# Performance work log

Hardware: AMD Instinct MI355X
Metric: run time of the kernel (lower is better)

Reference implementation:

```python
import jax, jax.numpy as jnp
import numpy as np
from jax import lax

# dims: B batch, L seq len, D channels, N SSM state size
BATCH, L, D, N = 8, 2048, 256, 64
MIN_DELTA = 1e-6
EPS = 1e-6


def setup_inputs() -> dict:
    key = jax.random.key(0)
    k0, k1, k2, k3, k4 = jax.random.split(key, 5)
    x = jax.random.normal(k0, (BATCH, L, D), dtype=jnp.float32)
    # log_A chosen so A = softplus(log_A) is small -> discrete_A^L stays finite in fp32
    log_A = -jax.random.normal(k1, (N, N), dtype=jnp.float32) - 3.0
    Bp = jax.random.normal(k2, (D, N), dtype=jnp.float32) * 0.02
    Cp = jax.random.normal(k3, (D, N), dtype=jnp.float32) * 0.02
    log_delta = jnp.full((D,), -8.0, dtype=jnp.float32)  # dt ~ 3.4e-4 (stability)
    skip_D = jnp.ones((D,), dtype=jnp.float32)
    W_out = jax.random.normal(k4, (D, D), dtype=jnp.float32) * (1.0 / np.sqrt(D))
    b_out = jnp.zeros((D,), dtype=jnp.float32)
    return dict(x=x, log_A=log_A, Bp=Bp, Cp=Cp, log_delta=log_delta,
                skip_D=skip_D, W_out=W_out, b_out=b_out)


def reference(x, log_A, Bp, Cp, log_delta, skip_D, W_out, b_out):
    Bsz, Lx, Dx = x.shape
    # --- discretize ---
    A = jax.nn.softplus(log_A)                                  # [N,N]
    dt = jax.nn.softplus(log_delta) + MIN_DELTA                 # [D]
    dA = jax.vmap(jax.scipy.linalg.expm)(A[None] * dt[:, None, None])  # [D,N,N]
    I = jnp.eye(A.shape[0], dtype=A.dtype)
    X = jnp.linalg.solve(A + EPS * I, Bp.T)                     # [N,D] = A^{-1} B^T
    dB = jnp.einsum('dnm,dm->dn', dA - I, X.T)                  # [D,N]
    # --- kernel k[d,l] = C_d . (dA_d)^l dB_d, via sequential recurrence (same math
    # as the explicit A-power loop, carrying the vector instead of the matrix) ---
    def step(v, _):
        return jnp.einsum('dnm,dm->dn', dA, v), jnp.sum(Cp * v, axis=-1)
    _, ks = lax.scan(step, dB, None, length=Lx)                 # ks: [L,D]
    k = ks.T                                                    # [D,L]
    # --- grouped causal conv1d: y[b,d,t] = sum_tau k[d,tau] x[b,d,t-tau] ---
    w = jnp.flip(k, -1)[:, None, :]                             # [D,1,L]
    y = lax.conv_general_dilated(
        jnp.transpose(x, (0, 2, 1)), w, (1,), [(Lx - 1, 0)],
        dimension_numbers=('NCH', 'OIH', 'NCH'), feature_group_count=Dx)
    y = jnp.transpose(y, (0, 2, 1))                             # [B,L,D]
    return (y + x * skip_D) @ W_out.T + b_out
```

## Files before the change

kernel.cpp:

```cpp
#include <hip/hip_runtime.h>

#define Bz 8
#define Lz 2048
#define Dz 256
#define Nz 64
#define SP 68
#define SA 65
#define SAK 72
#define SKB 136
#define KE 4
#define KP 7
#define BSP 4
#define BPB (Bz / BSP)

typedef __attribute__((ext_vector_type(8))) short bf16x8;
typedef __attribute__((ext_vector_type(4))) float f32x4;

__device__ __forceinline__ float softplusf(float x) {
  return (x > 20.f) ? x : log1pf(expf(x));
}

__device__ __forceinline__ unsigned short f2bf(float f) {
  unsigned int u = __float_as_uint(f);
  u += 0x7fffu + ((u >> 16) & 1u);
  return (unsigned short)(u >> 16);
}

__device__ __forceinline__ void pmm_acc(const float* __restrict__ LA,
                                        const float* __restrict__ LB,
                                        float* acc, int n, int q) {
  float arow[64];
#pragma unroll
  for (int mm = 0; mm < 16; ++mm) {
    const float4 a4 = *(const float4*)(LA + n * SP + mm * 4);
    arow[4 * mm + 0] = a4.x; arow[4 * mm + 1] = a4.y;
    arow[4 * mm + 2] = a4.z; arow[4 * mm + 3] = a4.w;
  }
#pragma unroll
  for (int i = 0; i < 16; ++i) acc[i] = 0.f;
#pragma unroll 8
  for (int m = 0; m < 64; ++m) {
    const float4 b0 = *(const float4*)(LB + m * SP + q * 16 + 0);
    const float4 b1 = *(const float4*)(LB + m * SP + q * 16 + 4);
    const float4 b2 = *(const float4*)(LB + m * SP + q * 16 + 8);
    const float4 b3 = *(const float4*)(LB + m * SP + q * 16 + 12);
    const float a = arow[m];
    acc[0]  = fmaf(a, b0.x, acc[0]);  acc[1]  = fmaf(a, b0.y, acc[1]);
    acc[2]  = fmaf(a, b0.z, acc[2]);  acc[3]  = fmaf(a, b0.w, acc[3]);
    acc[4]  = fmaf(a, b1.x, acc[4]);  acc[5]  = fmaf(a, b1.y, acc[5]);
    acc[6]  = fmaf(a, b1.z, acc[6]);  acc[7]  = fmaf(a, b1.w, acc[7]);
    acc[8]  = fmaf(a, b2.x, acc[8]);  acc[9]  = fmaf(a, b2.y, acc[9]);
    acc[10] = fmaf(a, b2.z, acc[10]); acc[11] = fmaf(a, b2.w, acc[11]);
    acc[12] = fmaf(a, b3.x, acc[12]); acc[13] = fmaf(a, b3.y, acc[13]);
    acc[14] = fmaf(a, b3.z, acc[14]); acc[15] = fmaf(a, b3.w, acc[15]);
  }
}

__global__ __launch_bounds__(256) void s4_xt(const float* __restrict__ x,
                                             float* __restrict__ xT,
                                             const float* __restrict__ log_A,
                                             float* __restrict__ Apow) {
  if (blockIdx.x == 0 && blockIdx.y == 0) {
    const int i = blockIdx.z * 512 + threadIdx.x;
    Apow[i] = softplusf(log_A[i]);
    Apow[i + 256] = softplusf(log_A[i + 256]);
  }
  __shared__ float tile[64][69];
  const int t0 = blockIdx.x * 64, d0 = blockIdx.y * 64, b = blockIdx.z;
  const int rr = threadIdx.x >> 4;
  const int c4 = (threadIdx.x & 15) * 4;
#pragma unroll
  for (int p = 0; p < 4; ++p) {
    const int row = p * 16 + rr;
    const float4 v = *(const float4*)(x + ((size_t)b * Lz + t0 + row) * Dz + d0 + c4);
    tile[row][c4 + 0] = v.x; tile[row][c4 + 1] = v.y;
    tile[row][c4 + 2] = v.z; tile[row][c4 + 3] = v.w;
  }
  __syncthreads();
#pragma unroll
  for (int p = 0; p < 4; ++p) {
    const int dd = p * 16 + rr;
    float4 o;
    o.x = tile[c4 + 0][dd]; o.y = tile[c4 + 1][dd];
    o.z = tile[c4 + 2][dd]; o.w = tile[c4 + 3][dd];
    *(float4*)(xT + ((size_t)(d0 + dd) * Bz + b) * Lz + t0 + c4) = o;
  }
}

__global__ __launch_bounds__(256, 1) void s4_buildpow(
    float* __restrict__ Apow, const float* __restrict__ Bp,
    const float* __restrict__ Cp, const float* __restrict__ log_delta,
    float* __restrict__ Gk, float* __restrict__ Qk,
    float* __restrict__ kloc, float* __restrict__ dts) {
  __shared__ float As[Nz * SA];
  __shared__ float Pst[KP + 1][Nz];
  __shared__ float Qst[KE + 1][Nz];
  __shared__ float Pv[Nz], Qv[Nz], dBs[Nz];
  __shared__ float prA[4][Nz + 8], prB[4][Nz + 8];
  __shared__ float zp[KE + 1][17], zs[KE + 1];
  __shared__ alignas(16) float PA[Nz * SP];
  __shared__ alignas(16) float PB[Nz * SP];
  const int tid = threadIdx.x;
  const int d = blockIdx.x;
  const int n = tid & 63, qq = tid >> 6;

  if (d >= Dz) {
    const int role = d - Dz;
#pragma unroll
    for (int i = 0; i < 4; ++i) {
      const int e = (tid + 256 * i) * 4;
      const int r = e >> 6, c = e & 63;
      const float4 v = *(const float4*)(Apow + e);
      *(float4*)&PA[r * SP + c] = v;
      *(float4*)&PB[r * SP + c] = v;
    }
    __syncthreads();
    float acc[16];
    pmm_acc(PA, PB, acc, n, qq);
    if (role == 0) {
      float* O = Apow + (size_t)1 * 4096;
#pragma unroll
      for (int v = 0; v < 4; ++v) {
        float4 o;
        o.x = acc[4 * v]; o.y = acc[4 * v + 1];
        o.z = acc[4 * v + 2]; o.w = acc[4 * v + 3];
        *(float4*)(O + n * 64 + qq * 16 + 4 * v) = o;
      }
      return;
    }
    __syncthreads();
#pragma unroll
    for (int i = 0; i < 16; ++i) {
      PB[n * SP + qq * 16 + i] = acc[i];
      if (role == 2) PA[n * SP + qq * 16 + i] = acc[i];
    }
    __syncthreads();
    pmm_acc(PA, PB, acc, n, qq);
    float* O = Apow + (size_t)(role + 1) * 4096;
#pragma unroll
    for (int v = 0; v < 4; ++v) {
      float4 o;
      o.x = acc[4 * v]; o.y = acc[4 * v + 1];
      o.z = acc[4 * v + 2]; o.w = acc[4 * v + 3];
      *(float4*)(O + n * 64 + qq * 16 + 4 * v) = o;
    }
    return;
  }

  const float dt = softplusf(log_delta[d]) + 1e-6f;
#pragma unroll
  for (int i = 0; i < 4; ++i) {
    const int e = (tid + 256 * i) * 4;
    const int r = e >> 6, c = e & 63;
    const float4 v = *(const float4*)(Apow + e);
    As[r * SA + c] = v.x; As[r * SA + c + 1] = v.y;
    As[r * SA + c + 2] = v.z; As[r * SA + c + 3] = v.w;
  }
  if (tid < 64) {
    const float bv = Bp[d * Nz + tid], cv = Cp[d * Nz + tid];
    Pv[tid] = bv; Pst[0][tid] = bv;
    Qv[tid] = cv; Qst[0][tid] = cv;
  }
  __syncthreads();
#pragma unroll 1
  for (int k = 1; k <= KP; ++k) {
    float pp = 0.f, pq = 0.f;
#pragma unroll
    for (int mm = 0; mm < 16; ++mm) {
      const int m = qq * 16 + mm;
      pp += As[n * SA + m] * Pv[m];
      pq += As[m * SA + n] * Qv[m];
    }
    prA[qq][n] = pp; prB[qq][n] = pq;
    __syncthreads();
    if (tid < 64) {
      const float np = prA[0][tid] + prA[1][tid] + prA[2][tid] + prA[3][tid];
      Pv[tid] = np; Pst[k][tid] = np;
      if (k <= KE) {
        const float nq = prB[0][tid] + prB[1][tid] + prB[2][tid] + prB[3][tid];
        Qv[tid] = nq; Qst[k][tid] = nq;
      }
    }
    __syncthreads();
  }
  const float dtc0 = dt;
  const float dtc1 = dt * dt * 0.5f;
  const float dtc2 = dtc1 * dt * (1.f / 3.f);
  const float dtc3 = dtc2 * dt * 0.25f;
  if (tid < 64) {
    dBs[tid] = dtc0 * Pst[0][tid] + dtc1 * Pst[1][tid] +
               dtc2 * Pst[2][tid] + dtc3 * Pst[3][tid];
#pragma unroll
    for (int k = 0; k <= KE; ++k) {
      Gk[(size_t)d * ((KE + 1) * 64) + k * 64 + tid] =
          dtc0 * Pst[k][tid] + dtc1 * Pst[k + 1][tid] +
          dtc2 * Pst[k + 2][tid] + dtc3 * Pst[k + 3][tid];
      Qk[(size_t)d * ((KE + 1) * 64) + k * 64 + tid] = Qst[k][tid];
    }
  }
  __syncthreads();
  if (tid < (KE + 1) * 16) {
    const int k = tid >> 4, seg = tid & 15;
    float s = 0.f;
#pragma unroll
    for (int i = 0; i < 4; ++i) s += Qst[k][seg * 4 + i] * dBs[seg * 4 + i];
    zp[k][seg] = s;
  }
  __syncthreads();
  if (tid <= KE) {
    float s = 0.f;
#pragma unroll
    for (int seg = 0; seg < 16; ++seg) s += zp[tid][seg];
    zs[tid] = s;
  }
  __syncthreads();
  if (tid < 64) {
    const float rdt = (float)tid * dt;
    float c = 1.f, acc = zs[0];
#pragma unroll
    for (int k = 1; k <= KE; ++k) { c *= rdt / (float)k; acc += c * zs[k]; }
    kloc[d * 64 + tid] = acc;
  }
  if (tid == 0) dts[d] = dt;
}

__global__ __launch_bounds__(256) void s4_scan5(
    const float* __restrict__ xT, const float* __restrict__ Apow,
    const float* __restrict__ Gk, const float* __restrict__ dts,
    float* __restrict__ S) {
  __shared__ float Es[Nz * SA];
  __shared__ float Gs[(KE + 1) * Nz];
  __shared__ float CTs[KE + 1][66];
  __shared__ alignas(16) float Xs[2][BPB][64];
  __shared__ alignas(16) float Ss[2][BPB][64];
  __shared__ float pr[4][BPB][64];
  const int d = blockIdx.x;
  const int z = blockIdx.y;
  const int tid = threadIdx.x, n = tid & 63, q = tid >> 6;
  const int rb = tid >> 6;
  const float dt = dts[d];
  if (tid < 65) {
    const float rdt = (float)tid * dt;
    float c = 1.f;
    CTs[0][tid] = 1.f;
#pragma unroll
    for (int k = 1; k <= KE; ++k) { c *= rdt / (float)k; CTs[k][tid] = c; }
  }
  for (int idx = tid; idx < (KE + 1) * 64; idx += 256)
    Gs[idx] = Gk[(size_t)d * ((KE + 1) * 64) + idx];
  {
    float ea[16];
#pragma unroll
    for (int i = 0; i < 16; ++i) ea[i] = 0.f;
    const float dt64 = 64.f * dt;
    float ce = 1.f;
#pragma unroll 1
    for (int k = 1; k <= KE; ++k) {
      ce *= dt64 / (float)k;
      const float* Ak = Apow + (size_t)(k - 1) * 4096;
#pragma unroll
      for (int i = 0; i < 16; ++i)
        ea[i] = fmaf(ce, Ak[tid + 256 * i], ea[i]);
    }
#pragma unroll
    for (int i = 0; i < 16; ++i) {
      const int e = tid + 256 * i;
      const int r = e >> 6, c = e & 63;
      Es[r * SA + c] = ea[i] + ((r == c) ? 1.f : 0.f);
    }
  }
  __syncthreads();
  float Er[16], Ur[16];
#pragma unroll
  for (int i = 0; i < 16; ++i) Er[i] = Es[n * SA + q * 16 + i];
#pragma unroll
  for (int i = 0; i < 16; ++i) {
    const int j = q * 16 + i;
    float u = 0.f;
#pragma unroll
    for (int k = 0; k <= KE; ++k) u = fmaf(CTs[k][63 - j], Gs[k * 64 + n], u);
    Ur[i] = u;
  }
  if (rb < BPB) Ss[0][rb][n] = 0.f;
  const float* xd = xT + ((size_t)d * Bz + z * BPB) * Lz;
  float* Sd = S + (size_t)d * (32 * 8 * 64) + (size_t)(z * BPB) * 64;
#pragma unroll 1
  for (int c = 0; c < 32; ++c) {
    const int cur = c & 1, nxt = cur ^ 1;
    if (rb < BPB) {
      Xs[cur][rb][n] = xd[(size_t)rb * Lz + c * 64 + n];
      Sd[c * 512 + rb * 64 + n] = Ss[cur][rb][n];
    }
    __syncthreads();
    float acc[BPB];
#pragma unroll
    for (int b = 0; b < BPB; ++b) {
      const float4 s0 = *(const float4*)&Ss[cur][b][q * 16 + 0];
      const float4 s1 = *(const float4*)&Ss[cur][b][q * 16 + 4];
      const float4 s2 = *(const float4*)&Ss[cur][b][q * 16 + 8];
      const float4 s3 = *(const float4*)&Ss[cur][b][q * 16 + 12];
      const float4 x0 = *(const float4*)&Xs[cur][b][q * 16 + 0];
      const float4 x1 = *(const float4*)&Xs[cur][b][q * 16 + 4];
      const float4 x2 = *(const float4*)&Xs[cur][b][q * 16 + 8];
      const float4 x3 = *(const float4*)&Xs[cur][b][q * 16 + 12];
      float a = 0.f;
      a = fmaf(Er[0], s0.x, a);  a = fmaf(Er[1], s0.y, a);
      a = fmaf(Er[2], s0.z, a);  a = fmaf(Er[3], s0.w, a);
      a = fmaf(Er[4], s1.x, a);  a = fmaf(Er[5], s1.y, a);
      a = fmaf(Er[6], s1.z, a);  a = fmaf(Er[7], s1.w, a);
      a = fmaf(Er[8], s2.x, a);  a = fmaf(Er[9], s2.y, a);
      a = fmaf(Er[10], s2.z, a); a = fmaf(Er[11], s2.w, a);
      a = fmaf(Er[12], s3.x, a); a = fmaf(Er[13], s3.y, a);
      a = fmaf(Er[14], s3.z, a); a = fmaf(Er[15], s3.w, a);
      a = fmaf(Ur[0], x0.x, a);  a = fmaf(Ur[1], x0.y, a);
      a = fmaf(Ur[2], x0.z, a);  a = fmaf(Ur[3], x0.w, a);
      a = fmaf(Ur[4], x1.x, a);  a = fmaf(Ur[5], x1.y, a);
      a = fmaf(Ur[6], x1.z, a);  a = fmaf(Ur[7], x1.w, a);
      a = fmaf(Ur[8], x2.x, a);  a = fmaf(Ur[9], x2.y, a);
      a = fmaf(Ur[10], x2.z, a); a = fmaf(Ur[11], x2.w, a);
      a = fmaf(Ur[12], x3.x, a); a = fmaf(Ur[13], x3.y, a);
      a = fmaf(Ur[14], x3.z, a); a = fmaf(Ur[15], x3.w, a);
      acc[b] = a;
    }
#pragma unroll
    for (int b = 0; b < BPB; ++b) pr[q][b][n] = acc[b];
    __syncthreads();
    if (rb < BPB)
      Ss[nxt][rb][n] = pr[0][rb][n] + pr[1][rb][n] + pr[2][rb][n] + pr[3][rb][n];
  }
}

__global__ __launch_bounds__(256, 4) void s4_out7(
    const float* __restrict__ xT, const float* __restrict__ S,
    const float* __restrict__ Qk, const float* __restrict__ kloc,
    const float* __restrict__ dts, const float* __restrict__ skip_D,
    unsigned short* __restrict__ yb) {
  __shared__ alignas(16) unsigned short Msb[64 * SKB];
  __shared__ alignas(16) unsigned short Zsb[64 * SKB];
  __shared__ float Qs[(KE + 1) * Nz];
  __shared__ float CT[KE + 1][66];
  __shared__ unsigned short kxb[64];
  const int d = blockIdx.x;
  const int ch = blockIdx.y;
  const int tid = threadIdx.x;
  const int wave = tid >> 6, lane = tid & 63;
  const int quad = lane >> 4, lq = lane & 15;
  const float dt = dts[d];
  if (tid < 65) {
    const float rdt = (float)tid * dt;
    float c = 1.f;
    CT[0][tid] = 1.f;
#pragma unroll
    for (int k = 1; k <= KE; ++k) { c *= rdt / (float)k; CT[k][tid] = c; }
  }
  for (int idx = tid; idx < (KE + 1) * 64; idx += 256)
    Qs[idx] = Qk[(size_t)d * ((KE + 1) * 64) + idx];
  if (tid < 64)
    kxb[tid] = f2bf(kloc[d * 64 + tid] + ((tid == 0) ? skip_D[d] : 0.f));

  const float* xd = xT + (size_t)d * Bz * Lz;
  const float* Sd = S + (size_t)d * (32 * 8 * 64);
#pragma unroll
  for (int p = 0; p < 8; ++p) {
    const int u = tid + 256 * p;
    const int col = u >> 5;
    const int sub = u & 31;
    const int k0 = sub * 4;
    const int bb = col & 7, ccl = col >> 3;
    const int cc = ch * 8 + ccl;
    const float* src = (k0 < 64)
        ? (Sd + cc * 512 + bb * 64 + k0)
        : (xd + (size_t)bb * Lz + cc * 64 + (k0 - 64));
    const float4 v = *(const float4*)src;
    ushort4 o;
    o.x = f2bf(v.x); o.y = f2bf(v.y); o.z = f2bf(v.z); o.w = f2bf(v.w);
    *(ushort4*)&Zsb[col * SKB + k0] = o;
  }
  __syncthreads();

#pragma unroll
  for (int i = 0; i < 16; ++i) {
    const int e = tid + 256 * i;
    const int r = e >> 6, m = e & 63;
    float w = 0.f;
#pragma unroll
    for (int k = 0; k <= KE; ++k) w = fmaf(CT[k][r + 1], Qs[k * 64 + m], w);
    Msb[r * SKB + m] = f2bf(w);
  }
#pragma unroll
  for (int i = 0; i < 16; ++i) {
    const int e = tid + 256 * i;
    const int r = e >> 6, j = e & 63;
    Msb[r * SKB + 64 + j] = (j <= r) ? kxb[r - j] : (unsigned short)0;
  }
  __syncthreads();

  f32x4 acc[4];
#pragma unroll
  for (int ni = 0; ni < 4; ++ni)
#pragma unroll
    for (int i = 0; i < 4; ++i) acc[ni][i] = 0.f;
#pragma unroll
  for (int ks = 0; ks < 4; ++ks) {
    const bf16x8 af =
        *(const bf16x8*)&Msb[(wave * 16 + lq) * SKB + ks * 32 + quad * 8];
#pragma unroll
    for (int ni = 0; ni < 4; ++ni) {
      const bf16x8 bfr =
          *(const bf16x8*)&Zsb[(ni * 16 + lq) * SKB + ks * 32 + quad * 8];
      acc[ni] = __builtin_amdgcn_mfma_f32_16x16x32_bf16(af, bfr, acc[ni], 0, 0, 0);
    }
  }
#pragma unroll
  for (int ni = 0; ni < 4; ++ni) {
    const int col = ni * 16 + lq;
    const int bb = col & 7, ccl = col >> 3;
    const int cc = ch * 8 + ccl;
    ushort4 o;
    o.x = f2bf(acc[ni][0]); o.y = f2bf(acc[ni][1]);
    o.z = f2bf(acc[ni][2]); o.w = f2bf(acc[ni][3]);
    *(ushort4*)(yb + ((size_t)d * Bz + bb) * Lz + cc * 64 + wave * 16 + quad * 4) = o;
  }
}

__global__ __launch_bounds__(256, 2) void s4_gemm5(
    const unsigned short* __restrict__ yb, const float* __restrict__ Wo,
    const float* __restrict__ bo, float* __restrict__ out) {
  __shared__ alignas(16) unsigned short LA[128 * SAK];
  __shared__ alignas(16) unsigned short LB[64 * SAK];
  const int tid = threadIdx.x;
  const int wave = tid >> 6, lane = tid & 63;
  const int quad = lane >> 4, lq = lane & 15;
  const int r0 = blockIdx.x * 128;
  const int c0 = blockIdx.y * 64;
  const int brow = r0 >> 11, t0 = r0 & 2047;
  const int ad = tid & 63;
  const int atg = tid >> 6;
  const int bc = tid >> 2;
  const int bko = tid & 3;
  f32x4 acc[2][4];
#pragma unroll
  for (int mi = 0; mi < 2; ++mi)
#pragma unroll
    for (int ni = 0; ni < 4; ++ni)
#pragma unroll
      for (int i = 0; i < 4; ++i) acc[mi][ni][i] = 0.f;
#pragma unroll 1
  for (int ks = 0; ks < 4; ++ks) {
    const int k0 = ks * 64;
    {
      const unsigned short* src =
          yb + ((size_t)(k0 + ad) * Bz + brow) * Lz + t0 + atg * 32;
#pragma unroll
      for (int h = 0; h < 4; ++h) {
        const bf16x8 v = *(const bf16x8*)(src + h * 8);
#pragma unroll
        for (int j = 0; j < 8; ++j)
          LA[(atg * 32 + h * 8 + j) * SAK + ad] = (unsigned short)v[j];
      }
    }
#pragma unroll
    for (int half = 0; half < 2; ++half) {
      const int kk = half * 32 + bko * 8;
      const float* wsrc = Wo + (size_t)(c0 + bc) * Dz + k0 + kk;
      const float4 w0 = *(const float4*)(wsrc);
      const float4 w1 = *(const float4*)(wsrc + 4);
      bf16x8 wv;
      wv[0] = (short)f2bf(w0.x); wv[1] = (short)f2bf(w0.y);
      wv[2] = (short)f2bf(w0.z); wv[3] = (short)f2bf(w0.w);
      wv[4] = (short)f2bf(w1.x); wv[5] = (short)f2bf(w1.y);
      wv[6] = (short)f2bf(w1.z); wv[7] = (short)f2bf(w1.w);
      *(bf16x8*)&LB[bc * SAK + kk] = wv;
    }
    __syncthreads();
#pragma unroll
    for (int ksub = 0; ksub < 2; ++ksub) {
      bf16x8 af[2], bfr[4];
#pragma unroll
      for (int mi = 0; mi < 2; ++mi)
        af[mi] = *(const bf16x8*)
            &LA[(wave * 32 + mi * 16 + lq) * SAK + ksub * 32 + quad * 8];
#pragma unroll
      for (int ni = 0; ni < 4; ++ni)
        bfr[ni] = *(const bf16x8*)
            &LB[(ni * 16 + lq) * SAK + ksub * 32 + quad * 8];
#pragma unroll
      for (int mi = 0; mi < 2; ++mi)
#pragma unroll
        for (int ni = 0; ni < 4; ++ni)
          acc[mi][ni] = __builtin_amdgcn_mfma_f32_16x16x32_bf16(
              af[mi], bfr[ni], acc[mi][ni], 0, 0, 0);
    }
    __syncthreads();
  }
  float bb[4];
#pragma unroll
  for (int ni = 0; ni < 4; ++ni) bb[ni] = bo[c0 + ni * 16 + lq];
#pragma unroll
  for (int mi = 0; mi < 2; ++mi)
#pragma unroll
    for (int i = 0; i < 4; ++i) {
      const int row = r0 + wave * 32 + mi * 16 + quad * 4 + i;
#pragma unroll
      for (int ni = 0; ni < 4; ++ni)
        out[(size_t)row * Dz + c0 + ni * 16 + lq] = acc[mi][ni][i] + bb[ni];
    }
}

extern "C" void kernel_launch(void* const* d_in, const int* in_sizes, int n_in,
                              void* d_out, int out_size, void* d_ws, size_t ws_size,
                              hipStream_t stream) {
  const float* x         = (const float*)d_in[0];
  const float* log_A     = (const float*)d_in[1];
  const float* Bp        = (const float*)d_in[2];
  const float* Cp        = (const float*)d_in[3];
  const float* log_delta = (const float*)d_in[4];
  const float* skip_D    = (const float*)d_in[5];
  const float* W_out     = (const float*)d_in[6];
  const float* b_out     = (const float*)d_in[7];
  float* out = (float*)d_out;

  float* xT   = (float*)d_ws;
  float* ybf  = xT + (size_t)Dz * Bz * Lz;
  float* S    = ybf + (size_t)Dz * Bz * Lz;
  float* Apow = S + (size_t)Dz * (32 * 8 * 64);
  float* Gk   = Apow + (size_t)8 * 4096;
  float* Qk   = Gk + (size_t)Dz * (KE + 1) * 64;
  float* kloc = Qk + (size_t)Dz * (KE + 1) * 64;
  float* dts  = kloc + (size_t)Dz * 64;
  unsigned short* yb = (unsigned short*)ybf;

  hipLaunchKernelGGL(s4_xt, dim3(Lz / 64, Dz / 64, Bz), dim3(256), 0, stream,
                     x, xT, log_A, Apow);
  hipLaunchKernelGGL(s4_buildpow, dim3(Dz + 3), dim3(256), 0, stream,
                     Apow, Bp, Cp, log_delta, Gk, Qk, kloc, dts);
  hipLaunchKernelGGL(s4_scan5, dim3(Dz, BSP), dim3(256), 0, stream,
                     xT, Apow, Gk, dts, S);
  hipLaunchKernelGGL(s4_out7, dim3(Dz, 4), dim3(256), 0, stream,
                     xT, S, Qk, kloc, dts, skip_D, yb);
  hipLaunchKernelGGL(s4_gemm5, dim3((Bz * Lz) / 128, Dz / 64), dim3(256), 0, stream,
                     yb, W_out, b_out, out);
}
```

Baseline: 150.1 us.

## Restructure chunk-state scan to one wave per batch with register-resident rows

The chunk-state scan kernel now uses one 512-thread block per channel, with each wave handling one batch element. Each lane holds a full row of the transition matrix and input matrix in registers, so the inner step needs no cross-wave partial-sum reduction and no block-wide barriers. x values are prefetched two chunks ahead, and the U matrix is precomputed into shared memory. The trade is heavy register use (128 floats of rows per thread), which may cause spills or low occupancy, and 256 blocks instead of 1024. It also relies on wave-synchronous shared-memory access without explicit barriers.

Measured after the change: 137.8 us (median of 2 runs). 8.2% less time.

```diff
diff --git a/kernel.cpp b/kernel.cpp
--- a/kernel.cpp
+++ b/kernel.cpp
@@ -8,10 +8,9 @@
 #define SA 65
 #define SAK 72
 #define SKB 136
+#define SE 68
 #define KE 4
 #define KP 7
-#define BSP 4
-#define BPB (Bz / BSP)
 
 typedef __attribute__((ext_vector_type(8))) short bf16x8;
 typedef __attribute__((ext_vector_type(4))) float f32x4;
@@ -224,20 +223,20 @@
   if (tid == 0) dts[d] = dt;
 }
 
-__global__ __launch_bounds__(256) void s4_scan5(
+__global__ __launch_bounds__(512, 2) void s4_scan7(
     const float* __restrict__ xT, const float* __restrict__ Apow,
     const float* __restrict__ Gk, const float* __restrict__ dts,
     float* __restrict__ S) {
-  __shared__ float Es[Nz * SA];
+  __shared__ alignas(16) float Es[Nz * SE];
+  __shared__ alignas(16) float Us[Nz * SE];
   __shared__ float Gs[(KE + 1) * Nz];
   __shared__ float CTs[KE + 1][66];
-  __shared__ alignas(16) float Xs[2][BPB][64];
-  __shared__ alignas(16) float Ss[2][BPB][64];
-  __shared__ float pr[4][BPB][64];
+  __shared__ alignas(16) float Sw[Bz][SE];
+  __shared__ alignas(16) float Xw[Bz][SE];
   const int d = blockIdx.x;
-  const int z = blockIdx.y;
-  const int tid = threadIdx.x, n = tid & 63, q = tid >> 6;
-  const int rb = tid >> 6;
+  const int tid = threadIdx.x;
+  const int w = tid >> 6;
+  const int n = tid & 63;
   const float dt = dts[d];
   if (tid < 65) {
     const float rdt = (float)tid * dt;
@@ -246,87 +245,87 @@
 #pragma unroll
     for (int k = 1; k <= KE; ++k) { c *= rdt / (float)k; CTs[k][tid] = c; }
   }
-  for (int idx = tid; idx < (KE + 1) * 64; idx += 256)
+  for (int idx = tid; idx < (KE + 1) * 64; idx += 512)
     Gs[idx] = Gk[(size_t)d * ((KE + 1) * 64) + idx];
   {
-    float ea[16];
-#pragma unroll
-    for (int i = 0; i < 16; ++i) ea[i] = 0.f;
+    float ea[8];
+#pragma unroll
+    for (int i = 0; i < 8; ++i) ea[i] = 0.f;
     const float dt64 = 64.f * dt;
     float ce = 1.f;
-#pragma unroll 1
+#pragma unroll
     for (int k = 1; k <= KE; ++k) {
       ce *= dt64 / (float)k;
       const float* Ak = Apow + (size_t)(k - 1) * 4096;
 #pragma unroll
-      for (int i = 0; i < 16; ++i)
-        ea[i] = fmaf(ce, Ak[tid + 256 * i], ea[i]);
-    }
-#pragma unroll
-    for (int i = 0; i < 16; ++i) {
-      const int e = tid + 256 * i;
+      for (int i = 0; i < 8; ++i)
+        ea[i] = fmaf(ce, Ak[tid + 512 * i], ea[i]);
+    }
+#pragma unroll
+    for (int i = 0; i < 8; ++i) {
+      const int e = tid + 512 * i;
       const int r = e >> 6, c = e & 63;
-      Es[r * SA + c] = ea[i] + ((r == c) ? 1.f : 0.f);
-    }
-  }
-  __syncthreads();
-  float Er[16], Ur[16];
-#pragma unroll
-  for (int i = 0; i < 16; ++i) Er[i] = Es[n * SA + q * 16 + i];
-#pragma unroll
-  for (int i = 0; i < 16; ++i) {
-    const int j = q * 16 + i;
-    float u = 0.f;
-#pragma unroll
-    for (int k = 0; k <= KE; ++k) u = fmaf(CTs[k][63 - j], Gs[k * 64 + n], u);
-    Ur[i] = u;
-  }
-  if (rb < BPB) Ss[0][rb][n] = 0.f;
-  const float* xd = xT + ((size_t)d * Bz + z * BPB) * Lz;
-  float* Sd = S + (size_t)d * (32 * 8 * 64) + (size_t)(z * BPB) * 64;
+      Es[r * SE + c] = ea[i] + ((r == c) ? 1.f : 0.f);
+    }
+  }
+  __syncthreads();
+  {
+    const int r = tid >> 3, j0 = (tid & 7) * 8;
+    float g0 = Gs[0 * 64 + r], g1 = Gs[1 * 64 + r], g2 = Gs[2 * 64 + r];
+    float g3 = Gs[3 * 64 + r], g4 = Gs[4 * 64 + r];
+#pragma unroll
+    for (int jj = 0; jj < 8; ++jj) {
+      const int j = j0 + jj;
+      float u = g0 * CTs[0][63 - j];
+      u = fmaf(g1, CTs[1][63 - j], u);
+      u = fmaf(g2, CTs[2][63 - j], u);
+      u = fmaf(g3, CTs[3][63 - j], u);
+      u = fmaf(g4, CTs[4][63 - j], u);
+      Us[r * SE + j] = u;
+    }
+  }
+  __syncthreads();
+  float Erow[64], Urow[64];
+#pragma unroll
+  for (int mb = 0; mb < 16; ++mb) {
+    const float4 e4 = *(const float4*)&Es[n * SE + 4 * mb];
+    Erow[4 * mb + 0] = e4.x; Erow[4 * mb + 1] = e4.y;
+    Erow[4 * mb + 2] = e4.z; Erow[4 * mb + 3] = e4.w;
+    const float4 u4 = *(const float4*)&Us[n * SE + 4 * mb];
+    Urow[4 * mb + 0] = u4.x; Urow[4 * mb + 1] = u4.y;
+    Urow[4 * mb + 2] = u4.z; Urow[4 * mb + 3] = u4.w;
+  }
+  const float* xw = xT + ((size_t)d * Bz + w) * (size_t)Lz;
+  float* Sd = S + (size_t)d * (32 * 8 * 64) + w * 64 + n;
+  float s = 0.f;
+  float xcur = xw[n];
+  float xnxt = xw[64 + n];
 #pragma unroll 1
   for (int c = 0; c < 32; ++c) {
-    const int cur = c & 1, nxt = cur ^ 1;
-    if (rb < BPB) {
-      Xs[cur][rb][n] = xd[(size_t)rb * Lz + c * 64 + n];
-      Sd[c * 512 + rb * 64 + n] = Ss[cur][rb][n];
-    }
-    __syncthreads();
-    float acc[BPB];
-#pragma unroll
-    for (int b = 0; b < BPB; ++b) {
-      const float4 s0 = *(const float4*)&Ss[cur][b][q * 16 + 0];
-      const float4 s1 = *(const float4*)&Ss[cur][b][q * 16 + 4];
-      const float4 s2 = *(const float4*)&Ss[cur][b][q * 16 + 8];
-      const float4 s3 = *(const float4*)&Ss[cur][b][q * 16 + 12];
-      const float4 x0 = *(const float4*)&Xs[cur][b][q * 16 + 0];
-      const float4 x1 = *(const float4*)&Xs[cur][b][q * 16 + 4];
-      const float4 x2 = *(const float4*)&Xs[cur][b][q * 16 + 8];
-      const float4 x3 = *(const float4*)&Xs[cur][b][q * 16 + 12];
-      float a = 0.f;
-      a = fmaf(Er[0], s0.x, a);  a = fmaf(Er[1], s0.y, a);
-      a = fmaf(Er[2], s0.z, a);  a = fmaf(Er[3], s0.w, a);
-      a = fmaf(Er[4], s1.x, a);  a = fmaf(Er[5], s1.y, a);
-      a = fmaf(Er[6], s1.z, a);  a = fmaf(Er[7], s1.w, a);
-      a = fmaf(Er[8], s2.x, a);  a = fmaf(Er[9], s2.y, a);
-      a = fmaf(Er[10], s2.z, a); a = fmaf(Er[11], s2.w, a);
-      a = fmaf(Er[12], s3.x, a); a = fmaf(Er[13], s3.y, a);
-      a = fmaf(Er[14], s3.z, a); a = fmaf(Er[15], s3.w, a);
-      a = fmaf(Ur[0], x0.x, a);  a = fmaf(Ur[1], x0.y, a);
-      a = fmaf(Ur[2], x0.z, a);  a = fmaf(Ur[3], x0.w, a);
-      a = fmaf(Ur[4], x1.x, a);  a = fmaf(Ur[5], x1.y, a);
-      a = fmaf(Ur[6], x1.z, a);  a = fmaf(Ur[7], x1.w, a);
-      a = fmaf(Ur[8], x2.x, a);  a = fmaf(Ur[9], x2.y, a);
-      a = fmaf(Ur[10], x2.z, a); a = fmaf(Ur[11], x2.w, a);
-      a = fmaf(Ur[12], x3.x, a); a = fmaf(Ur[13], x3.y, a);
-      a = fmaf(Ur[14], x3.z, a); a = fmaf(Ur[15], x3.w, a);
-      acc[b] = a;
-    }
-#pragma unroll
-    for (int b = 0; b < BPB; ++b) pr[q][b][n] = acc[b];
-    __syncthreads();
-    if (rb < BPB)
-      Ss[nxt][rb][n] = pr[0][rb][n] + pr[1][rb][n] + pr[2][rb][n] + pr[3][rb][n];
+    Sw[w][n] = s;
+    Xw[w][n] = xcur;
+    Sd[(size_t)c * 512] = s;
+    const int cl = (c + 2 < 32) ? (c + 2) : 31;
+    const float xnew = xw[cl * 64 + n];
+    float a0 = 0.f, a1 = 0.f, a2 = 0.f, a3 = 0.f;
+#pragma unroll
+    for (int mb = 0; mb < 16; ++mb) {
+      const float4 sb = *(const float4*)&Sw[w][4 * mb];
+      a0 = fmaf(Erow[4 * mb + 0], sb.x, a0);
+      a1 = fmaf(Erow[4 * mb + 1], sb.y, a1);
+      a2 = fmaf(Erow[4 * mb + 2], sb.z, a2);
+      a3 = fmaf(Erow[4 * mb + 3], sb.w, a3);
+    }
+#pragma unroll
+    for (int jb = 0; jb < 16; ++jb) {
+      const float4 xb = *(const float4*)&Xw[w][4 * jb];
+      a0 = fmaf(Urow[4 * jb + 0], xb.x, a0);
+      a1 = fmaf(Urow[4 * jb + 1], xb.y, a1);
+      a2 = fmaf(Urow[4 * jb + 2], xb.z, a2);
+      a3 = fmaf(Urow[4 * jb + 3], xb.w, a3);
+    }
+    s = (a0 + a1) + (a2 + a3);
+    xcur = xnxt; xnxt = xnew;
   }
 }
 
@@ -534,7 +533,7 @@
                      x, xT, log_A, Apow);
   hipLaunchKernelGGL(s4_buildpow, dim3(Dz + 3), dim3(256), 0, stream,
                      Apow, Bp, Cp, log_delta, Gk, Qk, kloc, dts);
-  hipLaunchKernelGGL(s4_scan5, dim3(Dz, BSP), dim3(256), 0, stream,
+  hipLaunchKernelGGL(s4_scan7, dim3(Dz), dim3(512), 0, stream,
                      xT, Apow, Gk, dts, S);
   hipLaunchKernelGGL(s4_out7, dim3(Dz, 4), dim3(256), 0, stream,
                      xT, S, Qk, kloc, dts, skip_D, yb);
```
